# Kernel tuning notes

Hardware: AMD Instinct MI355X
Metric: run time of the kernel (lower is better)

## Reference

```python
import jax, jax.numpy as jnp
import numpy as np


def _apply_rope(q, k):
    # q, k: [BH, T, hd]
    hd = q.shape[-1]
    half = hd // 2
    T = q.shape[1]
    inv_freq = 1.0 / (10000.0 ** (jnp.arange(half, dtype=jnp.float32) / half))
    freqs = jnp.arange(T, dtype=jnp.float32)[:, None] * inv_freq[None, :]  # [T, half]
    cos = jnp.cos(freqs)[None, :, :]
    sin = jnp.sin(freqs)[None, :, :]
    q1, q2 = q[..., :half], q[..., half:]
    k1, k2 = k[..., :half], k[..., half:]
    q_rot = jnp.concatenate([q1 * cos - q2 * sin, q1 * sin + q2 * cos], axis=-1)
    k_rot = jnp.concatenate([k1 * cos - k2 * sin, k1 * sin + k2 * cos], axis=-1)
    return q_rot, k_rot


def setup_inputs() -> dict:
    key = jax.random.key(0)
    ks = jax.random.split(key, 5)
    B, T, D = 2, 2048, 1024
    x = jax.random.normal(ks[0], (B, T, D), dtype=jnp.float32)
    w_qkv = jax.random.normal(ks[1], (D, 3 * D), dtype=jnp.float32) * (1.0 / np.sqrt(D))
    b_qkv = jax.random.normal(ks[2], (3 * D,), dtype=jnp.float32) * 0.01
    w_out = jax.random.normal(ks[3], (D, D), dtype=jnp.float32) * (1.0 / np.sqrt(D))
    b_out = jax.random.normal(ks[4], (D,), dtype=jnp.float32) * 0.01
    return {"x": x, "w_qkv": w_qkv, "b_qkv": b_qkv, "w_out": w_out, "b_out": b_out}


def reference(x, w_qkv, b_qkv, w_out, b_out):
    B, T, D = x.shape
    H = 16
    hd = D // H
    qkv = x @ w_qkv + b_qkv  # [B, T, 3D]
    q, k, v = jnp.split(qkv, 3, axis=-1)
    # [B, T, H, hd] -> [B, H, T, hd]
    q = q.reshape(B, T, H, hd).transpose(0, 2, 1, 3)
    k = k.reshape(B, T, H, hd).transpose(0, 2, 1, 3)
    v = v.reshape(B, T, H, hd).transpose(0, 2, 1, 3)
    q, k = _apply_rope(q.reshape(B * H, T, hd), k.reshape(B * H, T, hd))
    q = q.reshape(B, H, T, hd)
    k = k.reshape(B, H, T, hd)
    scores = jnp.einsum("bhqd,bhkd->bhqk", q, k) / jnp.sqrt(jnp.float32(hd))
    attn = jax.nn.softmax(scores, axis=-1)
    out = jnp.einsum("bhqk,bhkd->bhqd", attn, v)  # [B, H, T, hd]
    out = out.transpose(0, 2, 1, 3).reshape(B, T, D)
    return out @ w_out + b_out
```

## Files before the change

kernel.cpp:

```cpp
#include <hip/hip_runtime.h>
#include <hip/hip_bf16.h>
#include <stdint.h>


typedef __bf16 bf16;
typedef __bf16 bf16x8 __attribute__((ext_vector_type(8)));
typedef __bf16 bf16x4 __attribute__((ext_vector_type(4)));
typedef short  s16x4  __attribute__((ext_vector_type(4)));
typedef float  f32x4  __attribute__((ext_vector_type(4)));

__device__ __forceinline__ void gload16(void* lds, const void* g) {
  __builtin_amdgcn_global_load_lds((__attribute__((address_space(1))) void*)(void*)g,
                                   (__attribute__((address_space(3))) void*)lds, 16, 0, 0);
}

__device__ __forceinline__ f32x4 mfma16x16x16(bf16x4 a, bf16x4 b, f32x4 c) {
  return __builtin_amdgcn_mfma_f32_16x16x16bf16_1k(
      __builtin_bit_cast(s16x4, a), __builtin_bit_cast(s16x4, b), c, 0, 0, 0);
}


__global__ void k_convert_x(const float* __restrict__ x, bf16* __restrict__ xb, int n) {
  int i = (blockIdx.x * blockDim.x + threadIdx.x) * 4;
  if (i >= n) return;
  float4 v = *(const float4*)(x + i);
  bf16x4 o;
  o.x = (bf16)v.x; o.y = (bf16)v.y; o.z = (bf16)v.z; o.w = (bf16)v.w;
  *(bf16x4*)(xb + i) = o;
}

__global__ void k_transpose_bf16(const float* __restrict__ in, bf16* __restrict__ out,
                                 int rows, int cols) {
  __shared__ float t[32][33];
  int c0 = blockIdx.x * 32, r0 = blockIdx.y * 32;
  for (int i = threadIdx.y; i < 32; i += 8)
    t[i][threadIdx.x] = in[(size_t)(r0 + i) * cols + c0 + threadIdx.x];
  __syncthreads();
  for (int i = threadIdx.y; i < 32; i += 8)
    out[(size_t)(c0 + i) * rows + r0 + threadIdx.x] = (bf16)t[threadIdx.x][i];
}


__global__ __launch_bounds__(256)
void k_gemm_qkv(const bf16* __restrict__ A, const bf16* __restrict__ Bt,
                const float* __restrict__ bias, bf16* __restrict__ Qd,
                bf16* __restrict__ Kd, bf16* __restrict__ Vtd) {
  alignas(16) __shared__ bf16 lds_a[128 * 32];
  alignas(16) __shared__ bf16 lds_b[128 * 32];
  const int tid = threadIdx.x;
  const int lane = tid & 63, w = tid >> 6;
  const int wr = w >> 1, wc = w & 1;
  const int bid = blockIdx.x;
  const int swz = (bid & 7) * 96 + (bid >> 3);
  const int br = swz / 24, bc = swz % 24;
  const int r16 = lane & 15, g4 = lane >> 4;

  f32x4 acc[4][4] = {};
  const bf16* gA = A + (size_t)(br * 128 + (lane >> 2)) * 1024 + (lane & 3) * 8;
  const bf16* gB = Bt + (size_t)(bc * 128 + (lane >> 2)) * 1024 + (lane & 3) * 8;

  for (int kt = 0; kt < 32; ++kt) {
    const int ko = kt * 32;
#pragma unroll
    for (int it = 0; it < 2; ++it) {
      const int row0 = 16 * (4 * it + w);
      gload16(&lds_a[row0 * 32], gA + (size_t)row0 * 1024 + ko);
      gload16(&lds_b[row0 * 32], gB + (size_t)row0 * 1024 + ko);
    }
    __syncthreads();
    bf16x8 af[4], bfr[4];
#pragma unroll
    for (int m = 0; m < 4; ++m)
      af[m] = *(const bf16x8*)&lds_a[(wr * 64 + 16 * m + r16) * 32 + g4 * 8];
#pragma unroll
    for (int n = 0; n < 4; ++n)
      bfr[n] = *(const bf16x8*)&lds_b[(wc * 64 + 16 * n + r16) * 32 + g4 * 8];
#pragma unroll
    for (int m = 0; m < 4; ++m)
#pragma unroll
      for (int n = 0; n < 4; ++n)
        acc[m][n] = __builtin_amdgcn_mfma_f32_16x16x32_bf16(af[m], bfr[n], acc[m][n], 0, 0, 0);
    __syncthreads();
  }

  const int reg = bc >> 3;
  const int h = ((bc & 7) << 1) | wc;
  const float bq = 0.125f * 1.4426950408889634f;
  const float Lc = 13.287712379549449f / 32.0f;
  const float if0 = exp2f(-(float)r16 * Lc);
  const float if1 = exp2f(-(float)(16 + r16) * Lc);
  float bv[4];
#pragma unroll
  for (int n = 0; n < 4; ++n) bv[n] = bias[bc * 128 + wc * 64 + 16 * n + r16];

  if (reg == 2) {
#pragma unroll
    for (int m = 0; m < 4; ++m) {
      const int row0 = br * 128 + wr * 64 + 16 * m + 4 * g4;
      const int t0 = row0 & 2047, b = row0 >> 11;
      const int pos = (t0 & ~63) | (((t0 >> 2) & 3) << 4) | (((t0 >> 5) & 1) << 3) |
                      (((t0 >> 4) & 1) << 2);
#pragma unroll
      for (int n = 0; n < 4; ++n) {
        bf16x4 pk;
#pragma unroll
        for (int r = 0; r < 4; ++r) pk[r] = (bf16)(acc[m][n][r] + bv[n]);
        *(bf16x4*)(Vtd + ((size_t)((b * 16 + h) * 64) + 16 * n + r16) * 2048 + pos) = pk;
      }
    }
  } else {
    bf16* dst = (reg == 0) ? Qd : Kd;
#pragma unroll
    for (int m = 0; m < 4; ++m) {
#pragma unroll
      for (int r = 0; r < 4; ++r) {
        const int row = br * 128 + wr * 64 + 16 * m + 4 * g4 + r;
        const int t = row & 2047, b = row >> 11;
        bf16* o = dst + ((size_t)(b * 16 + h) * 2048 + t) * 64;
        const float v0 = acc[m][0][r] + bv[0];
        const float v1 = acc[m][1][r] + bv[1];
        const float v2 = acc[m][2][r] + bv[2];
        const float v3 = acc[m][3][r] + bv[3];
        float s0, c0, s1, c1;
        const float tf = (float)t;
        sincosf(tf * if0, &s0, &c0);
        sincosf(tf * if1, &s1, &c1);
        float r0 = v0 * c0 - v2 * s0, r2 = v0 * s0 + v2 * c0;
        float r1 = v1 * c1 - v3 * s1, r3 = v1 * s1 + v3 * c1;
        if (reg == 0) { r0 *= bq; r1 *= bq; r2 *= bq; r3 *= bq; }
        o[r16]      = (bf16)r0;
        o[16 + r16] = (bf16)r1;
        o[32 + r16] = (bf16)r2;
        o[48 + r16] = (bf16)r3;
      }
    }
  }
}


__global__ __launch_bounds__(256)
void k_gemm_out(const bf16* __restrict__ A, const bf16* __restrict__ Bt,
                const float* __restrict__ bias, float* __restrict__ Cp,
                int M, int N, int K) {
  alignas(16) __shared__ bf16 lds_a[128 * 32];
  alignas(16) __shared__ bf16 lds_b[128 * 32];
  const int tid = threadIdx.x;
  const int lane = tid & 63, w = tid >> 6;
  const int wr = w >> 1, wc = w & 1;
  const int nb = N >> 7;
  const int nwg = gridDim.x;
  const int bid = blockIdx.x;
  const int swz = (bid & 7) * (nwg >> 3) + (bid >> 3);
  const int br = swz / nb, bc = swz % nb;
  const int r16 = lane & 15, g4 = lane >> 4;

  f32x4 acc[4][4] = {};
  const int nk = K >> 5;
  const bf16* gA = A + (size_t)(br * 128 + (lane >> 2)) * K + (lane & 3) * 8;
  const bf16* gB = Bt + (size_t)(bc * 128 + (lane >> 2)) * K + (lane & 3) * 8;

  for (int kt = 0; kt < nk; ++kt) {
    const int ko = kt * 32;
#pragma unroll
    for (int it = 0; it < 2; ++it) {
      const int row0 = 16 * (4 * it + w);
      gload16(&lds_a[row0 * 32], gA + (size_t)row0 * K + ko);
      gload16(&lds_b[row0 * 32], gB + (size_t)row0 * K + ko);
    }
    __syncthreads();
    bf16x8 af[4], bfr[4];
#pragma unroll
    for (int m = 0; m < 4; ++m)
      af[m] = *(const bf16x8*)&lds_a[(wr * 64 + 16 * m + r16) * 32 + g4 * 8];
#pragma unroll
    for (int n = 0; n < 4; ++n)
      bfr[n] = *(const bf16x8*)&lds_b[(wc * 64 + 16 * n + r16) * 32 + g4 * 8];
#pragma unroll
    for (int m = 0; m < 4; ++m)
#pragma unroll
      for (int n = 0; n < 4; ++n)
        acc[m][n] = __builtin_amdgcn_mfma_f32_16x16x32_bf16(af[m], bfr[n], acc[m][n], 0, 0, 0);
    __syncthreads();
  }

#pragma unroll
  for (int m = 0; m < 4; ++m) {
    const int row = br * 128 + wr * 64 + 16 * m + 4 * g4;
#pragma unroll
    for (int n = 0; n < 4; ++n) {
      const int col = bc * 128 + wc * 64 + 16 * n + r16;
      const float bvv = bias[col];
#pragma unroll
      for (int r = 0; r < 4; ++r)
        Cp[(size_t)(row + r) * N + col] = acc[m][n][r] + bvv;
    }
  }
}


__global__ __launch_bounds__(256)
void k_attn(const bf16* __restrict__ Qg, const bf16* __restrict__ Kg,
            const bf16* __restrict__ Vtg, bf16* __restrict__ Og) {
  alignas(16) __shared__ bf16 kbuf[2][4096];
  alignas(16) __shared__ bf16 vbuf[2][4096];
  const int tid = threadIdx.x, lane = tid & 63, w = tid >> 6;
  const int bid = blockIdx.x;
  const int swz = (bid & 7) * 128 + (bid >> 3);
  const int bh = swz >> 5, q0 = (swz & 31) * 64;
  const int r16 = lane & 15, g4 = lane >> 4;
  const char* Kb  = (const char*)(Kg  + (size_t)bh * 2048 * 64);
  const char* Vtb = (const char*)(Vtg + (size_t)bh * 64 * 2048);
  const bf16* Qb  = Qg + (size_t)bh * 2048 * 64;

  const int rl = lane >> 3;
  const int colx = ((lane & 7) * 16) ^ (rl << 4);

  bf16x8 qf[2];
  {
    const int qrow = q0 + 16 * w + r16;
    qf[0] = *(const bf16x8*)(Qb + (size_t)qrow * 64 + g4 * 8);
    qf[1] = *(const bf16x8*)(Qb + (size_t)qrow * 64 + 32 + g4 * 8);
  }

  f32x4 O[4] = {};
  f32x4 O4 = {};
  float m = -1e30f;
  bf16x4 ones = {};
  if (r16 == 0) { ones[0] = (bf16)1.f; ones[1] = (bf16)1.f; ones[2] = (bf16)1.f; ones[3] = (bf16)1.f; }

#define STAGE(bufi, t0)                                                          \
  {                                                                              \
    _Pragma("unroll")                                                            \
    for (int c = 0; c < 2; ++c) {                                                \
      const int row = 16 * w + 8 * c + rl;                                       \
      gload16(&kbuf[bufi][(2 * w + c) * 512],                                    \
              Kb + (size_t)((t0) + row) * 128 + colx);                           \
      gload16(&vbuf[bufi][(2 * w + c) * 512],                                    \
              Vtb + (size_t)row * 4096 + (size_t)(t0) * 2 + colx);               \
    }                                                                            \
  }

  STAGE(0, 0);
  __syncthreads();

  const int rsw = (r16 & 7) << 4;

#pragma unroll 1
  for (int it = 0; it < 32; ++it) {
    const int bsel = it & 1;
    if (it + 1 < 32) STAGE(bsel ^ 1, (it + 1) * 64);
    const char* kb = (const char*)kbuf[bsel] + r16 * 128;
    const char* vb = (const char*)vbuf[bsel] + r16 * 128;

    f32x4 S[4];
#pragma unroll
    for (int n = 0; n < 4; ++n) {
      bf16x8 kb0 = *(const bf16x8*)(kb + n * 2048 + ((g4 * 16) ^ rsw));
      bf16x8 kb1 = *(const bf16x8*)(kb + n * 2048 + ((64 + g4 * 16) ^ rsw));
      f32x4 s = {};
      s = __builtin_amdgcn_mfma_f32_16x16x32_bf16(kb0, qf[0], s, 0, 0, 0);
      s = __builtin_amdgcn_mfma_f32_16x16x32_bf16(kb1, qf[1], s, 0, 0, 0);
      S[n] = s;
    }

    float pmax = fmaxf(
        fmaxf(fmaxf(fmaxf(S[0][0], S[0][1]), S[0][2]),
              fmaxf(fmaxf(S[0][3], S[1][0]), S[1][1])),
        fmaxf(fmaxf(fmaxf(S[1][2], S[1][3]), S[2][0]),
              fmaxf(fmaxf(S[2][1], S[2][2]), S[2][3])));
    pmax = fmaxf(pmax, fmaxf(fmaxf(S[3][0], S[3][1]), fmaxf(S[3][2], S[3][3])));

    if (!__all(pmax - m <= 8.0f)) {
      float gmax = pmax;
      gmax = fmaxf(gmax, __shfl_xor(gmax, 16, 64));
      gmax = fmaxf(gmax, __shfl_xor(gmax, 32, 64));
      const float mn = fmaxf(m, gmax);
      const float alpha = exp2f(m - mn);
      m = mn;
#pragma unroll
      for (int n = 0; n < 4; ++n)
#pragma unroll
        for (int r = 0; r < 4; ++r) O[n][r] *= alpha;
      O4[0] *= alpha;
    }

    bf16x4 pb[4];
#pragma unroll
    for (int n = 0; n < 4; ++n)
#pragma unroll
      for (int r = 0; r < 4; ++r) pb[n][r] = (bf16)exp2f(S[n][r] - m);

#pragma unroll
    for (int dn = 0; dn < 4; ++dn) {
      bf16x8 v0 = *(const bf16x8*)(vb + dn * 2048 + ((32 * g4) ^ rsw));
      bf16x8 v1 = *(const bf16x8*)(vb + dn * 2048 + ((32 * g4 + 16) ^ rsw));
      O[dn] = mfma16x16x16(__builtin_shufflevector(v0, v0, 0, 1, 2, 3), pb[0], O[dn]);
      O[dn] = mfma16x16x16(__builtin_shufflevector(v0, v0, 4, 5, 6, 7), pb[1], O[dn]);
      O[dn] = mfma16x16x16(__builtin_shufflevector(v1, v1, 0, 1, 2, 3), pb[2], O[dn]);
      O[dn] = mfma16x16x16(__builtin_shufflevector(v1, v1, 4, 5, 6, 7), pb[3], O[dn]);
    }
#pragma unroll
    for (int kn = 0; kn < 4; ++kn) O4 = mfma16x16x16(ones, pb[kn], O4);
    __syncthreads();
  }
#undef STAGE

  const float ls = __shfl(O4[0], r16, 64);
  const float inv = 1.f / ls;
  const int b = bh >> 4, h = bh & 15;
  const int t = q0 + 16 * w + r16;
#pragma unroll
  for (int n = 0; n < 4; ++n) {
    bf16x4 ov;
#pragma unroll
    for (int r = 0; r < 4; ++r) ov[r] = (bf16)(O[n][r] * inv);
    *(bf16x4*)(Og + ((size_t)(b * 2048 + t)) * 1024 + h * 64 + 16 * n + 4 * g4) = ov;
  }
}


extern "C" void kernel_launch(void* const* d_in, const int* in_sizes, int n_in,
                              void* d_out, int out_size, void* d_ws, size_t ws_size,
                              hipStream_t stream) {
  const float* x     = (const float*)d_in[0];
  const float* w_qkv = (const float*)d_in[1];
  const float* b_qkv = (const float*)d_in[2];
  const float* w_out = (const float*)d_in[3];
  const float* b_out = (const float*)d_in[4];
  float* out = (float*)d_out;

  char* ws = (char*)d_ws;
  bf16* xb    = (bf16*)(ws);
  bf16* wqkvT = (bf16*)(ws + 8388608);
  bf16* woutT = (bf16*)(ws + 14680064);
  bf16* Qb    = (bf16*)(ws + 16777216);
  bf16* Kb    = (bf16*)(ws + 25165824);
  bf16* Vtb   = (bf16*)(ws + 33554432);
  bf16* attnb = (bf16*)(ws + 41943040);

  k_convert_x<<<4096 * 1024 / 4 / 256, 256, 0, stream>>>(x, xb, 4096 * 1024);
  k_transpose_bf16<<<dim3(3072 / 32, 1024 / 32), dim3(32, 8), 0, stream>>>(w_qkv, wqkvT, 1024, 3072);
  k_transpose_bf16<<<dim3(1024 / 32, 1024 / 32), dim3(32, 8), 0, stream>>>(w_out, woutT, 1024, 1024);
  k_gemm_qkv<<<32 * 24, 256, 0, stream>>>(xb, wqkvT, b_qkv, Qb, Kb, Vtb);
  k_attn<<<1024, 256, 0, stream>>>(Qb, Kb, Vtb, attnb);
  k_gemm_out<<<32 * 8, 256, 0, stream>>>(attnb, woutT, b_out, out, 4096, 1024, 1024);
}
```

Before: 153.4 us.

## Process two query tiles per attention block and use 16x16x32 MFMA for PV

Each attention block now handles 128 query rows (two 64-row groups per wave set) instead of 64, so every staged K/V tile in LDS feeds twice as many MFMAs and the grid halves to 512 blocks. The PV and row-sum products switch from 16x16x16 to 16x16x32 MFMAs with packed 8-wide P fragments, halving the instruction count. The cost is doubled accumulator and score registers per thread, which may lower occupancy, and fewer blocks to spread across CUs.

```diff
diff --git a/kernel.cpp b/kernel.cpp
--- a/kernel.cpp
+++ b/kernel.cpp
@@ -12,11 +12,6 @@
 __device__ __forceinline__ void gload16(void* lds, const void* g) {
   __builtin_amdgcn_global_load_lds((__attribute__((address_space(1))) void*)(void*)g,
                                    (__attribute__((address_space(3))) void*)lds, 16, 0, 0);
-}
-
-__device__ __forceinline__ f32x4 mfma16x16x16(bf16x4 a, bf16x4 b, f32x4 c) {
-  return __builtin_amdgcn_mfma_f32_16x16x16bf16_1k(
-      __builtin_bit_cast(s16x4, a), __builtin_bit_cast(s16x4, b), c, 0, 0, 0);
 }
 
 
@@ -205,8 +200,8 @@
   alignas(16) __shared__ bf16 vbuf[2][4096];
   const int tid = threadIdx.x, lane = tid & 63, w = tid >> 6;
   const int bid = blockIdx.x;
-  const int swz = (bid & 7) * 128 + (bid >> 3);
-  const int bh = swz >> 5, q0 = (swz & 31) * 64;
+  const int swz = (bid & 7) * 64 + (bid >> 3);
+  const int bh = swz >> 4, q0 = (swz & 15) * 128;
   const int r16 = lane & 15, g4 = lane >> 4;
   const char* Kb  = (const char*)(Kg  + (size_t)bh * 2048 * 64);
   const char* Vtb = (const char*)(Vtg + (size_t)bh * 64 * 2048);
@@ -215,18 +210,21 @@
   const int rl = lane >> 3;
   const int colx = ((lane & 7) * 16) ^ (rl << 4);
 
-  bf16x8 qf[2];
-  {
-    const int qrow = q0 + 16 * w + r16;
-    qf[0] = *(const bf16x8*)(Qb + (size_t)qrow * 64 + g4 * 8);
-    qf[1] = *(const bf16x8*)(Qb + (size_t)qrow * 64 + 32 + g4 * 8);
-  }
-
-  f32x4 O[4] = {};
-  f32x4 O4 = {};
-  float m = -1e30f;
-  bf16x4 ones = {};
-  if (r16 == 0) { ones[0] = (bf16)1.f; ones[1] = (bf16)1.f; ones[2] = (bf16)1.f; ones[3] = (bf16)1.f; }
+  bf16x8 qf[2][2];
+#pragma unroll
+  for (int g = 0; g < 2; ++g) {
+    const int qrow = q0 + 64 * g + 16 * w + r16;
+    qf[g][0] = *(const bf16x8*)(Qb + (size_t)qrow * 64 + g4 * 8);
+    qf[g][1] = *(const bf16x8*)(Qb + (size_t)qrow * 64 + 32 + g4 * 8);
+  }
+
+  f32x4 O[2][4] = {};
+  f32x4 O4[2] = {};
+  float m0 = -1e30f, m1 = -1e30f;
+  bf16x8 ones8 = {};
+  if (r16 == 0)
+#pragma unroll
+    for (int j = 0; j < 8; ++j) ones8[j] = (bf16)1.f;
 
 #define STAGE(bufi, t0)                                                          \
   {                                                                              \
@@ -252,69 +250,89 @@
     const char* kb = (const char*)kbuf[bsel] + r16 * 128;
     const char* vb = (const char*)vbuf[bsel] + r16 * 128;
 
-    f32x4 S[4];
+    f32x4 S0[4], S1[4];
 #pragma unroll
     for (int n = 0; n < 4; ++n) {
       bf16x8 kb0 = *(const bf16x8*)(kb + n * 2048 + ((g4 * 16) ^ rsw));
       bf16x8 kb1 = *(const bf16x8*)(kb + n * 2048 + ((64 + g4 * 16) ^ rsw));
       f32x4 s = {};
-      s = __builtin_amdgcn_mfma_f32_16x16x32_bf16(kb0, qf[0], s, 0, 0, 0);
-      s = __builtin_amdgcn_mfma_f32_16x16x32_bf16(kb1, qf[1], s, 0, 0, 0);
-      S[n] = s;
-    }
-
-    float pmax = fmaxf(
-        fmaxf(fmaxf(fmaxf(S[0][0], S[0][1]), S[0][2]),
-              fmaxf(fmaxf(S[0][3], S[1][0]), S[1][1])),
-        fmaxf(fmaxf(fmaxf(S[1][2], S[1][3]), S[2][0]),
-              fmaxf(fmaxf(S[2][1], S[2][2]), S[2][3])));
-    pmax = fmaxf(pmax, fmaxf(fmaxf(S[3][0], S[3][1]), fmaxf(S[3][2], S[3][3])));
-
-    if (!__all(pmax - m <= 8.0f)) {
-      float gmax = pmax;
-      gmax = fmaxf(gmax, __shfl_xor(gmax, 16, 64));
-      gmax = fmaxf(gmax, __shfl_xor(gmax, 32, 64));
-      const float mn = fmaxf(m, gmax);
-      const float alpha = exp2f(m - mn);
-      m = mn;
+      s = __builtin_amdgcn_mfma_f32_16x16x32_bf16(kb0, qf[0][0], s, 0, 0, 0);
+      s = __builtin_amdgcn_mfma_f32_16x16x32_bf16(kb1, qf[0][1], s, 0, 0, 0);
+      S0[n] = s;
+      f32x4 t = {};
+      t = __builtin_amdgcn_mfma_f32_16x16x32_bf16(kb0, qf[1][0], t, 0, 0, 0);
+      t = __builtin_amdgcn_mfma_f32_16x16x32_bf16(kb1, qf[1][1], t, 0, 0, 0);
+      S1[n] = t;
+    }
+
+    float pmax0 = fmaxf(
+        fmaxf(fmaxf(fmaxf(S0[0][0], S0[0][1]), S0[0][2]),
+              fmaxf(fmaxf(S0[0][3], S0[1][0]), S0[1][1])),
+        fmaxf(fmaxf(fmaxf(S0[1][2], S0[1][3]), S0[2][0]),
+              fmaxf(fmaxf(S0[2][1], S0[2][2]), S0[2][3])));
+    pmax0 = fmaxf(pmax0, fmaxf(fmaxf(S0[3][0], S0[3][1]), fmaxf(S0[3][2], S0[3][3])));
+    float pmax1 = fmaxf(
+        fmaxf(fmaxf(fmaxf(S1[0][0], S1[0][1]), S1[0][2]),
+              fmaxf(fmaxf(S1[0][3], S1[1][0]), S1[1][1])),
+        fmaxf(fmaxf(fmaxf(S1[1][2], S1[1][3]), S1[2][0]),
+              fmaxf(fmaxf(S1[2][1], S1[2][2]), S1[2][3])));
+    pmax1 = fmaxf(pmax1, fmaxf(fmaxf(S1[3][0], S1[3][1]), fmaxf(S1[3][2], S1[3][3])));
+
+    if (!__all(fmaxf(pmax0 - m0, pmax1 - m1) <= 8.0f)) {
+      float gm0 = pmax0, gm1 = pmax1;
+      gm0 = fmaxf(gm0, __shfl_xor(gm0, 16, 64));
+      gm0 = fmaxf(gm0, __shfl_xor(gm0, 32, 64));
+      gm1 = fmaxf(gm1, __shfl_xor(gm1, 16, 64));
+      gm1 = fmaxf(gm1, __shfl_xor(gm1, 32, 64));
+      const float mn0 = fmaxf(m0, gm0), mn1 = fmaxf(m1, gm1);
+      const float a0 = exp2f(m0 - mn0), a1 = exp2f(m1 - mn1);
+      m0 = mn0; m1 = mn1;
 #pragma unroll
       for (int n = 0; n < 4; ++n)
 #pragma unroll
-        for (int r = 0; r < 4; ++r) O[n][r] *= alpha;
-      O4[0] *= alpha;
-    }
-
-    bf16x4 pb[4];
+        for (int r = 0; r < 4; ++r) { O[0][n][r] *= a0; O[1][n][r] *= a1; }
+      O4[0][0] *= a0; O4[1][0] *= a1;
+    }
+
+    bf16x8 pb0[2], pb1[2];
 #pragma unroll
     for (int n = 0; n < 4; ++n)
 #pragma unroll
-      for (int r = 0; r < 4; ++r) pb[n][r] = (bf16)exp2f(S[n][r] - m);
+      for (int r = 0; r < 4; ++r) {
+        pb0[n >> 1][(n & 1) * 4 + r] = (bf16)exp2f(S0[n][r] - m0);
+        pb1[n >> 1][(n & 1) * 4 + r] = (bf16)exp2f(S1[n][r] - m1);
+      }
 
 #pragma unroll
     for (int dn = 0; dn < 4; ++dn) {
       bf16x8 v0 = *(const bf16x8*)(vb + dn * 2048 + ((32 * g4) ^ rsw));
       bf16x8 v1 = *(const bf16x8*)(vb + dn * 2048 + ((32 * g4 + 16) ^ rsw));
-      O[dn] = mfma16x16x16(__builtin_shufflevector(v0, v0, 0, 1, 2, 3), pb[0], O[dn]);
-      O[dn] = mfma16x16x16(__builtin_shufflevector(v0, v0, 4, 5, 6, 7), pb[1], O[dn]);
-      O[dn] = mfma16x16x16(__builtin_shufflevector(v1, v1, 0, 1, 2, 3), pb[2], O[dn]);
-      O[dn] = mfma16x16x16(__builtin_shufflevector(v1, v1, 4, 5, 6, 7), pb[3], O[dn]);
-    }
-#pragma unroll
-    for (int kn = 0; kn < 4; ++kn) O4 = mfma16x16x16(ones, pb[kn], O4);
+      O[0][dn] = __builtin_amdgcn_mfma_f32_16x16x32_bf16(v0, pb0[0], O[0][dn], 0, 0, 0);
+      O[0][dn] = __builtin_amdgcn_mfma_f32_16x16x32_bf16(v1, pb0[1], O[0][dn], 0, 0, 0);
+      O[1][dn] = __builtin_amdgcn_mfma_f32_16x16x32_bf16(v0, pb1[0], O[1][dn], 0, 0, 0);
+      O[1][dn] = __builtin_amdgcn_mfma_f32_16x16x32_bf16(v1, pb1[1], O[1][dn], 0, 0, 0);
+    }
+    O4[0] = __builtin_amdgcn_mfma_f32_16x16x32_bf16(ones8, pb0[0], O4[0], 0, 0, 0);
+    O4[0] = __builtin_amdgcn_mfma_f32_16x16x32_bf16(ones8, pb0[1], O4[0], 0, 0, 0);
+    O4[1] = __builtin_amdgcn_mfma_f32_16x16x32_bf16(ones8, pb1[0], O4[1], 0, 0, 0);
+    O4[1] = __builtin_amdgcn_mfma_f32_16x16x32_bf16(ones8, pb1[1], O4[1], 0, 0, 0);
     __syncthreads();
   }
 #undef STAGE
 
-  const float ls = __shfl(O4[0], r16, 64);
-  const float inv = 1.f / ls;
   const int b = bh >> 4, h = bh & 15;
-  const int t = q0 + 16 * w + r16;
-#pragma unroll
-  for (int n = 0; n < 4; ++n) {
-    bf16x4 ov;
-#pragma unroll
-    for (int r = 0; r < 4; ++r) ov[r] = (bf16)(O[n][r] * inv);
-    *(bf16x4*)(Og + ((size_t)(b * 2048 + t)) * 1024 + h * 64 + 16 * n + 4 * g4) = ov;
+#pragma unroll
+  for (int g = 0; g < 2; ++g) {
+    const float ls = __shfl(O4[g][0], r16, 64);
+    const float inv = 1.f / ls;
+    const int t = q0 + 64 * g + 16 * w + r16;
+#pragma unroll
+    for (int n = 0; n < 4; ++n) {
+      bf16x4 ov;
+#pragma unroll
+      for (int r = 0; r < 4; ++r) ov[r] = (bf16)(O[g][n][r] * inv);
+      *(bf16x4*)(Og + ((size_t)(b * 2048 + t)) * 1024 + h * 64 + 16 * n + 4 * g4) = ov;
+    }
   }
 }
 
@@ -342,6 +360,6 @@
   k_transpose_bf16<<<dim3(3072 / 32, 1024 / 32), dim3(32, 8), 0, stream>>>(w_qkv, wqkvT, 1024, 3072);
   k_transpose_bf16<<<dim3(1024 / 32, 1024 / 32), dim3(32, 8), 0, stream>>>(w_out, woutT, 1024, 1024);
   k_gemm_qkv<<<32 * 24, 256, 0, stream>>>(xb, wqkvT, b_qkv, Qb, Kb, Vtb);
-  k_attn<<<1024, 256, 0, stream>>>(Qb, Kb, Vtb, attnb);
+  k_attn<<<512, 256, 0, stream>>>(Qb, Kb, Vtb, attnb);
   k_gemm_out<<<32 * 8, 256, 0, stream>>>(attnb, woutT, b_out, out, 4096, 1024, 1024);
 }
```

Result: faster. 146.9 us (-4.2%).
